# Kernel optimization log

Measured on AMD Instinct MI355X. Metric: run time of the kernel, lower is better.

## Reference

```python
import jax, jax.numpy as jnp
import numpy as np

THRESH = 0.5
TAU = 0.5
GAMMA = 1.0
BETA = 0.9
A = 0.5
B = 0.5


def zif_spike(v):
    # ZIF surrogate: forward is hard threshold (v > 0).
    return (v > 0).astype(v.dtype)


def setup_inputs() -> dict:
    key = jax.random.key(0)
    x = jax.random.normal(key, (64, 8192, 100), dtype=jnp.float32)
    return {"x": x}


def reference(x):
    # x: [B, N, T]; scan over time with (mem, w) state kept per element.
    xt = jnp.moveaxis(x, 2, 0)  # [T, B, N]
    init_mem = jnp.zeros(xt.shape[1:], dtype=x.dtype)
    init_w = jnp.zeros(xt.shape[1:], dtype=x.dtype)

    def step(carry, x_t):
        mem, w = carry
        mem = mem * TAU + x_t - w
        spike = zif_spike(mem - THRESH)
        w = BETA * w + (1.0 - BETA) * (A * mem + B * spike)
        mem = mem - spike * THRESH  # soft reset
        return (mem, w), spike

    _, spikes = jax.lax.scan(step, (init_mem, init_w), xt)  # [T, B, N]
    return jnp.moveaxis(spikes, 0, 2)  # [B, N, T]
```

## Files before the change

### kernel.cpp

```cpp
#include <hip/hip_runtime.h>

#define T_STEPS 100
#define CHUNKS 25

__global__ __launch_bounds__(256) void lif_kernel(const float* __restrict__ x,
                                                  float* __restrict__ out,
                                                  int n_elem) {
#pragma clang fp contract(off)
    int e = blockIdx.x * blockDim.x + threadIdx.x;
    if (e >= n_elem) return;

    const float4* __restrict__ xp = (const float4*)(x + (size_t)e * T_STEPS);
    float4* __restrict__ op = (float4*)(out + (size_t)e * T_STEPS);

    float4 xs[CHUNKS];
#pragma unroll
    for (int c = 0; c < CHUNKS; ++c) xs[c] = xp[c];

    float mem = 0.0f;
    float w = 0.0f;

#pragma unroll
    for (int c = 0; c < CHUNKS; ++c) {
        float xv[4] = {xs[c].x, xs[c].y, xs[c].z, xs[c].w};
        float sv[4];
#pragma unroll
        for (int j = 0; j < 4; ++j) {
            mem = (mem * 0.5f + xv[j]) - w;
            float spike = (mem - 0.5f) > 0.0f ? 1.0f : 0.0f;
            w = 0.9f * w + 0.1f * (0.5f * mem + 0.5f * spike);
            mem = mem - spike * 0.5f;
            sv[j] = spike;
        }
        float4 s;
        s.x = sv[0]; s.y = sv[1]; s.z = sv[2]; s.w = sv[3];
        op[c] = s;
    }
}

extern "C" void kernel_launch(void* const* d_in, const int* in_sizes, int n_in,
                              void* d_out, int out_size, void* d_ws, size_t ws_size,
                              hipStream_t stream) {
    const float* x = (const float*)d_in[0];
    float* out = (float*)d_out;
    int n_elem = in_sizes[0] / T_STEPS;

    const int block = 256;
    const int grid = (n_elem + block - 1) / block;
    lif_kernel<<<grid, block, 0, stream>>>(x, out, n_elem);
}
```

Baseline: 417.4 us.

## Stage time series through swizzled LDS tile for coalesced global loads and stores

Each block now loads a 128-element by 100-step tile with fully coalesced float4 reads into shared memory, using an XOR swizzle to limit bank conflicts. Each thread then runs its recurrence from LDS and writes spikes back in place, and the block stores the tile with coalesced writes. Before, each thread read 400 contiguous bytes, so accesses across a wavefront were strided by row. In exchange the kernel uses 64KB of LDS per block and adds two barriers, which lowers occupancy. The tail guard is gone, so the element count must be a multiple of 128.

```diff
diff --git a/kernel.cpp b/kernel.cpp
--- a/kernel.cpp
+++ b/kernel.cpp
@@ -1,40 +1,71 @@
 #include <hip/hip_runtime.h>
 
 #define T_STEPS 100
-#define CHUNKS 25
+#define CHUNKS  25
+#define ELEMS   128
+#define TPB     128
+#define ROW4    32
 
-__global__ __launch_bounds__(256) void lif_kernel(const float* __restrict__ x,
-                                                  float* __restrict__ out,
-                                                  int n_elem) {
+__device__ __forceinline__ int slot(int e, int c) {
+    return e * ROW4 + (c ^ (e & 7));
+}
+
+__global__ __launch_bounds__(TPB) void lif_kernel(const float* __restrict__ x,
+                                                  float* __restrict__ out) {
 #pragma clang fp contract(off)
-    int e = blockIdx.x * blockDim.x + threadIdx.x;
-    if (e >= n_elem) return;
+    __shared__ float4 tile[ELEMS * ROW4];
 
-    const float4* __restrict__ xp = (const float4*)(x + (size_t)e * T_STEPS);
-    float4* __restrict__ op = (float4*)(out + (size_t)e * T_STEPS);
+    const int tid = threadIdx.x;
+    const size_t tile4 = (size_t)blockIdx.x * (ELEMS * CHUNKS);
+    const float4* __restrict__ xb = (const float4*)x + tile4;
+    float4* __restrict__ ob = (float4*)out + tile4;
 
-    float4 xs[CHUNKS];
+    {
+        int e = tid / 25;
+        int c = tid - e * 25;
 #pragma unroll
-    for (int c = 0; c < CHUNKS; ++c) xs[c] = xp[c];
+        for (int k = 0; k < CHUNKS; ++k) {
+            float4 v = xb[k * TPB + tid];
+            tile[slot(e, c)] = v;
+            c += 3; e += 5;
+            if (c >= CHUNKS) { c -= CHUNKS; e += 1; }
+        }
+    }
+    __syncthreads();
 
-    float mem = 0.0f;
-    float w = 0.0f;
+    {
+        float mem = 0.0f;
+        float w = 0.0f;
+#pragma unroll
+        for (int c = 0; c < CHUNKS; ++c) {
+            float4 xv4 = tile[slot(tid, c)];
+            float xv[4] = {xv4.x, xv4.y, xv4.z, xv4.w};
+            float sv[4];
+#pragma unroll
+            for (int j = 0; j < 4; ++j) {
+                mem = (mem * 0.5f + xv[j]) - w;
+                float spike = (mem - 0.5f) > 0.0f ? 1.0f : 0.0f;
+                w = 0.9f * w + 0.1f * (0.5f * mem + 0.5f * spike);
+                mem = mem - spike * 0.5f;
+                sv[j] = spike;
+            }
+            float4 s4;
+            s4.x = sv[0]; s4.y = sv[1]; s4.z = sv[2]; s4.w = sv[3];
+            tile[slot(tid, c)] = s4;
+        }
+    }
+    __syncthreads();
 
+    {
+        int e = tid / 25;
+        int c = tid - e * 25;
 #pragma unroll
-    for (int c = 0; c < CHUNKS; ++c) {
-        float xv[4] = {xs[c].x, xs[c].y, xs[c].z, xs[c].w};
-        float sv[4];
-#pragma unroll
-        for (int j = 0; j < 4; ++j) {
-            mem = (mem * 0.5f + xv[j]) - w;
-            float spike = (mem - 0.5f) > 0.0f ? 1.0f : 0.0f;
-            w = 0.9f * w + 0.1f * (0.5f * mem + 0.5f * spike);
-            mem = mem - spike * 0.5f;
-            sv[j] = spike;
+        for (int k = 0; k < CHUNKS; ++k) {
+            float4 s = tile[slot(e, c)];
+            ob[k * TPB + tid] = s;
+            c += 3; e += 5;
+            if (c >= CHUNKS) { c -= CHUNKS; e += 1; }
         }
-        float4 s;
-        s.x = sv[0]; s.y = sv[1]; s.z = sv[2]; s.w = sv[3];
-        op[c] = s;
     }
 }
 
@@ -44,8 +75,7 @@
     const float* x = (const float*)d_in[0];
     float* out = (float*)d_out;
     int n_elem = in_sizes[0] / T_STEPS;
+    int grid = n_elem / ELEMS;
 
-    const int block = 256;
-    const int grid = (n_elem + block - 1) / block;
-    lif_kernel<<<grid, block, 0, stream>>>(x, out, n_elem);
+    lif_kernel<<<grid, TPB, 0, stream>>>(x, out);
 }
```

Result: faster. 350.8 us (-16.0%).
